# Kernel tuning notes

Measured on AMD Instinct MI355X. Metric: run time of the kernel, lower is better.

Reference implementation:

```python
import jax, jax.numpy as jnp
import numpy as np
import math

B, S, D = 4, 2048, 1024
H, HD, L = 16, 64, 512
ROPE_BASE = 10000.0
EPS = 1e-6


def _rope_angles(seq_len, head_dim, base):
    # (seq_len, head_dim//2) rotation angles
    inv_freq = 1.0 / (base ** (jnp.arange(0, head_dim, 2, dtype=jnp.float32) / head_dim))
    pos = jnp.arange(seq_len, dtype=jnp.float32)
    return pos[:, None] * inv_freq[None, :]


def _apply_rope(t, ang):
    # t: (B, H, S, HD); half-split rotation (rotate-half convention)
    cos = jnp.cos(ang)  # (S, HD//2)
    sin = jnp.sin(ang)
    t1, t2 = jnp.split(t, 2, axis=-1)
    return jnp.concatenate([t1 * cos - t2 * sin, t1 * sin + t2 * cos], axis=-1)


def setup_inputs() -> dict:
    key = jax.random.key(0)
    ks = jax.random.split(key, 7)
    def w(k, shape, fan_in):
        return jax.random.normal(k, shape, jnp.float32) * (fan_in ** -0.5)
    return {
        "x": jax.random.normal(ks[0], (B, S, D), jnp.float32),
        "norm_w": jnp.ones((D,), jnp.float32),
        "wq": w(ks[1], (D, H * HD), D),
        "kv_down": w(ks[2], (D, L), D),
        "wk": w(ks[3], (L, H * HD), L),
        "wv": w(ks[4], (L, H * HD), L),
        "wo": w(ks[5], (H * HD, D), H * HD),
    }


def reference(x, norm_w, wq, kv_down, wk, wv, wo):
    residual = x
    # RMSNorm
    var = jnp.mean(x * x, axis=-1, keepdims=True)
    xn = x * jax.lax.rsqrt(var + EPS) * norm_w
    # Projections: q from full x, k/v from latent down-projection
    q = (xn @ wq).reshape(B, S, H, HD).transpose(0, 2, 1, 3)          # (B,H,S,HD)
    kv = xn @ kv_down                                                  # (B,S,L)
    k = (kv @ wk).reshape(B, S, H, HD).transpose(0, 2, 1, 3)
    v = (kv @ wv).reshape(B, S, H, HD).transpose(0, 2, 1, 3)
    # RoPE
    ang = _rope_angles(S, HD, ROPE_BASE)
    q = _apply_rope(q, ang)
    k = _apply_rope(k, ang)
    # Attention (full, no mask)
    scale = 1.0 / math.sqrt(HD)
    attn = jnp.einsum("bhsd,bhtd->bhst", q, k) * scale
    attn = jax.nn.softmax(attn, axis=-1)
    out = jnp.einsum("bhst,bhtd->bhsd", attn, v)
    out = out.transpose(0, 2, 1, 3).reshape(B, S, H * HD) @ wo
    return residual + out
```

## Files before the change

### kernel.cpp

```cpp
#include <hip/hip_runtime.h>

typedef unsigned short u16;
typedef unsigned int   u32;
typedef __attribute__((ext_vector_type(8)))  __bf16 bf16x8;
typedef __attribute__((ext_vector_type(2)))  __bf16 bf16x2;
typedef __attribute__((ext_vector_type(8)))  short  short8;
typedef __attribute__((ext_vector_type(4)))  float  f32x4;
typedef __attribute__((ext_vector_type(16))) float  f32x16;
typedef __attribute__((ext_vector_type(4)))  u16    u16x4;
typedef __attribute__((ext_vector_type(4)))  u32    u32x4;

#define DEV static __device__ __forceinline__

DEV u16 f2bf(float f){ return __builtin_bit_cast(u16, (__bf16)f); }
DEV u32 pkbf(float a, float b){ bf16x2 t; t[0] = (__bf16)a; t[1] = (__bf16)b;
                                return __builtin_bit_cast(u32, t); }

#if __has_builtin(__builtin_amdgcn_exp2f)
DEV float fexp2(float x){ return __builtin_amdgcn_exp2f(x); }
#else
DEV float fexp2(float x){ return exp2f(x); }
#endif

DEV f32x4 mfma16(short8 a, short8 b, f32x4 c){
  return __builtin_amdgcn_mfma_f32_16x16x32_bf16(
      __builtin_bit_cast(bf16x8, a), __builtin_bit_cast(bf16x8, b), c, 0, 0, 0);
}
DEV f32x16 mfma32(short8 a, short8 b, f32x16 c){
  return __builtin_amdgcn_mfma_f32_32x32x16_bf16(
      __builtin_bit_cast(bf16x8, a), __builtin_bit_cast(bf16x8, b), c, 0, 0, 0);
}
DEV int swz(int byteoff, int row){ return byteoff ^ ((row & 7) << 4); }

#if __has_builtin(__builtin_amdgcn_global_load_lds)
#define USE_GLL 1
typedef __attribute__((address_space(1))) const u32 gas_u32;
typedef __attribute__((address_space(3)))       u32 las_u32;
#define GL2L(g, l) __builtin_amdgcn_global_load_lds((gas_u32*)(g), (las_u32*)(l), 16, 0, 0)
#define LSWZ(boff, r) swz(boff, r)
#else
#define LSWZ(boff, r) (boff)
#endif

__global__ __launch_bounds__(256) void k_prep(const float* __restrict__ wq,
                                              const float* __restrict__ kvd,
                                              const float* __restrict__ wk,
                                              const float* __restrict__ wv,
                                              const float* __restrict__ wo,
                                              const float* __restrict__ x,
                                              const float* __restrict__ norm_w,
                                              u16* __restrict__ wqT, u16* __restrict__ kvdT,
                                              u16* __restrict__ wkT, u16* __restrict__ wvT,
                                              u16* __restrict__ woT, u16* __restrict__ xn,
                                              float2* __restrict__ cs, float qscale){
  const int z = blockIdx.z;
  if (z == 6){
    const int bid = blockIdx.y*32 + blockIdx.x;
    const int t = threadIdx.x;
    __shared__ float ps[4];
    const float4 g = ((const float4*)norm_w)[t];
    #pragma unroll 1
    for (int it = 0; it < 8; ++it){
      const int row = bid*8 + it;
      const float4 v = ((const float4*)(x + (size_t)row*1024))[t];
      float ss = v.x*v.x + v.y*v.y + v.z*v.z + v.w*v.w;
      #pragma unroll
      for (int off=32; off; off>>=1) ss += __shfl_xor(ss, off, 64);
      if ((t & 63) == 0) ps[t>>6] = ss;
      __syncthreads();
      const float tot = ps[0]+ps[1]+ps[2]+ps[3];
      const float rinv = rsqrtf(tot * (1.0f/1024.0f) + 1e-6f);
      u16x4 o;
      o.x = f2bf(v.x*rinv*g.x); o.y = f2bf(v.y*rinv*g.y);
      o.z = f2bf(v.z*rinv*g.z); o.w = f2bf(v.w*rinv*g.w);
      *(u16x4*)(xn + (size_t)row*1024 + t*4) = o;
      __syncthreads();
    }
    return;
  }
  if (z == 5){
    if (blockIdx.y >= 8) return;
    const int idx = (blockIdx.y*32 + blockIdx.x)*256 + threadIdx.x;
    const int s = idx >> 5, j = idx & 31;
    const float ang = (float)s * expf(-(float)j * (9.210340371976184f/32.0f));
    cs[idx] = make_float2(cosf(ang), sinf(ang));
    return;
  }
  const float* W; u16* Wt; int K, N; float sc = 1.0f;
  switch (z){
    case 0: W = wq;  Wt = wqT;  K = 1024; N = 1024; sc = qscale; break;
    case 1: W = kvd; Wt = kvdT; K = 1024; N = 512;  break;
    case 2: W = wk;  Wt = wkT;  K = 512;  N = 1024; break;
    case 3: W = wv;  Wt = wvT;  K = 512;  N = 1024; break;
    default: W = wo; Wt = woT;  K = 1024; N = 1024; break;
  }
  const int k0 = blockIdx.x*32, n0 = blockIdx.y*32;
  if (k0 >= K || n0 >= N) return;
  __shared__ float t[32][33];
  const int tx = threadIdx.x & 31, ty = threadIdx.x >> 5;
  #pragma unroll
  for (int j=0;j<4;++j) t[ty + j*8][tx] = W[(size_t)(k0+ty+j*8)*N + n0 + tx];
  __syncthreads();
  #pragma unroll
  for (int j=0;j<4;++j) Wt[(size_t)(n0+ty+j*8)*K + k0 + tx] = f2bf(t[tx][ty+j*8]*sc);
}

template<int MODE>
__global__ __launch_bounds__(256) void k_gemm(const u16* __restrict__ A,
                                              const u16* __restrict__ Bt,
                                              const u16* __restrict__ Bt2,
                                              u16* __restrict__ Cb,
                                              u16* __restrict__ Cb2,
                                              float* __restrict__ Cf,
                                              const float* __restrict__ resid,
                                              const float2* __restrict__ cs,
                                              int K){
  __shared__ __align__(16) u16 Al[2][128*64];
  __shared__ __align__(16) u16 Bl[2][128*64];
  const int tid = threadIdx.x, lane = tid & 63, w = tid >> 6;
  const int wm = (w >> 1) * 64, wn = (w & 1) * 64;

  const int gx = gridDim.x;
  const int nwg = gx * gridDim.y;
  int fid = blockIdx.y * gx + blockIdx.x;
  fid = (fid & 7) * (nwg >> 3) + (fid >> 3);
  const int bx = fid % gx, by = fid / gx;

  const bool second = (MODE != 2) && (bx >= 8);
  const u16* B = second ? Bt2 : Bt;
  const int n0 = (second ? bx - 8 : bx) * 128;
  const int m0 = by * 128;
  const int lr = lane & 15, lg = lane >> 4;
  const int nt = K >> 6;

  f32x4 acc[4][4] = {};

#ifdef USE_GLL
  const int rin  = lane >> 3;
  const int colq = (lane & 7) ^ rin;
  auto stage = [&](int t_){
    u16* Ad = &Al[t_ & 1][0];
    u16* Bd = &Bl[t_ & 1][0];
    const int kb = t_ << 6;
    #pragma unroll
    for (int j=0;j<4;++j){
      const int c = w*4 + j;
      GL2L(A + (size_t)(m0 + c*8 + rin)*K + kb + colq*8, Ad + c*512);
      GL2L(B + (size_t)(n0 + c*8 + rin)*K + kb + colq*8, Bd + c*512);
    }
  };
#else
  auto stage = [&](int t_){
    u16* Ad = &Al[t_ & 1][0];
    u16* Bd = &Bl[t_ & 1][0];
    const int kb = t_ << 6;
    const int srow = tid >> 1, scol = (tid & 1) * 32;
    #pragma unroll
    for (int j=0;j<4;++j){
      *(short8*)(Ad + srow*64 + scol + j*8) = *(const short8*)(A + (size_t)(m0+srow)*K + kb + scol + j*8);
      *(short8*)(Bd + srow*64 + scol + j*8) = *(const short8*)(B + (size_t)(n0+srow)*K + kb + scol + j*8);
    }
  };
#endif

  stage(0);
  for (int t = 0; t < nt; ++t){
    __syncthreads();
    if (t + 1 < nt) stage(t + 1);
    const u16* Ab = &Al[t & 1][0];
    const u16* Bb = &Bl[t & 1][0];
    #pragma unroll
    for (int kk=0; kk<2; ++kk){
      const int cb = kk*64 + lg*16;
      short8 af[4], bfr[4];
      #pragma unroll
      for (int m=0;m<4;++m){
        const int r = wm + m*16 + lr;
        af[m] = *(const short8*)((const char*)Ab + LSWZ(r*128 + cb, r));
      }
      #pragma unroll
      for (int n=0;n<4;++n){
        const int r = wn + n*16 + lr;
        bfr[n] = *(const short8*)((const char*)Bb + LSWZ(r*128 + cb, r));
      }
      #pragma unroll
      for (int m=0;m<4;++m)
        #pragma unroll
        for (int n=0;n<4;++n)
          acc[m][n] = mfma16(af[m], bfr[n], acc[m][n]);
    }
  }

  #pragma unroll
  for (int m=0;m<4;++m){
    const int rb = m0 + wm + m*16 + lg*4;
    if (MODE == 2){
      #pragma unroll
      for (int n=0;n<4;++n){
        const int c = n0 + wn + n*16 + lr;
        #pragma unroll
        for (int i=0;i<4;++i){
          const size_t off = (size_t)(rb+i)*1024 + c;
          Cf[off] = acc[m][n][i] + resid[off];
        }
      }
    } else if (!second){
      #pragma unroll
      for (int n=0;n<2;++n){
        const int c = n0 + wn + n*16 + lr;
        const int j = n*16 + lr;
        #pragma unroll
        for (int i=0;i<4;++i){
          const float2 t = cs[(size_t)((rb+i) & 2047)*32 + j];
          const float t1 = acc[m][n][i], t2 = acc[m][n+2][i];
          Cb[(size_t)(rb+i)*1024 + c]      = f2bf(t1*t.x - t2*t.y);
          Cb[(size_t)(rb+i)*1024 + c + 32] = f2bf(t1*t.y + t2*t.x);
        }
      }
    } else if (MODE == 4){
      #pragma unroll
      for (int n=0;n<4;++n){
        const int c = n0 + wn + n*16 + lr;
        #pragma unroll
        for (int i=0;i<4;++i) Cb2[(size_t)(rb+i)*512 + c] = f2bf(acc[m][n][i]);
      }
    } else {
      #pragma unroll
      for (int n=0;n<4;++n){
        const int c = n0 + wn + n*16 + lr;
        const int b = rb >> 11, s = rb & 2047;
        u16x4 pk;
        pk.x = f2bf(acc[m][n][0]); pk.y = f2bf(acc[m][n][1]);
        pk.z = f2bf(acc[m][n][2]); pk.w = f2bf(acc[m][n][3]);
        *(u16x4*)(Cb2 + (((size_t)(b*1024 + c)) << 11) + s) = pk;
      }
    }
  }
}

__global__ __launch_bounds__(512, 4) void k_attn(const u16* __restrict__ q,
                                                 const u16* __restrict__ kmat,
                                                 const u16* __restrict__ vT,
                                                 u16* __restrict__ o){
  __shared__ __align__(16) u16 Kl[2][64*64];
  __shared__ __align__(16) u16 Vl[2][64*64];
  const int tid = threadIdx.x, lane = tid & 63, w = tid >> 6;
  const int l31 = lane & 31, hi = lane >> 5;

  const int fid = blockIdx.y * 8 + blockIdx.x;
  const int sid = (fid & 7) * 64 + (fid >> 3);
  const int qx = sid & 7, bh = sid >> 3;
  const int b = bh >> 4, h = bh & 15;
  const int q0 = qx * 256;

  short8 qf[4];
  {
    const size_t base = ((size_t)(b*2048 + q0 + w*32 + l31) << 10) + (h<<6) + hi*8;
    qf[0] = *(const short8*)(q + base);
    qf[1] = *(const short8*)(q + base + 16);
    qf[2] = *(const short8*)(q + base + 32);
    qf[3] = *(const short8*)(q + base + 48);
  }
  f32x16 oacc0 = {}, oacc1 = {};
  f32x16 accl  = {};
  float m = -1e30f;
  const short8 ones = {0x3F80,0x3F80,0x3F80,0x3F80,0x3F80,0x3F80,0x3F80,0x3F80};

  int roff[8];
  #pragma unroll
  for (int c=0;c<4;++c){
    roff[c*2+0] = swz(l31*128      + c*32 + hi*16, l31);
    roff[c*2+1] = swz((32+l31)*128 + c*32 + hi*16, 32+l31);
  }

  const int rin  = lane >> 3;
  const int colq = (lane & 7) ^ rin;
  const u16* kp0 = kmat + ((size_t)(b*2048 + w*8 + rin) << 10) + (h<<6) + colq*8;
  const u16* vp0 = vT + (((size_t)(b*1024 + h*64 + w*8 + rin)) << 11) + colq*8;
  u16* const Kd0 = Kl[0] + w*512;  u16* const Kd1 = Kl[1] + w*512;
  u16* const Vd0 = Vl[0] + w*512;  u16* const Vd1 = Vl[1] + w*512;

#ifdef USE_GLL
  #define STAGE(KD, VD) { GL2L(kp0, KD); GL2L(vp0, VD);                         \
      kp0 += 65536; vp0 += 64; }
#else
  #define STAGE(KD, VD) { *(short8*)(KD + lane*8) = *(const short8*)(kp0);      \
      *(short8*)(VD + lane*8) = *(const short8*)(vp0);                          \
      kp0 += 65536; vp0 += 64; }
#endif

  #define TILE(BOFF) {                                                          \
    f32x16 s0 = {}, s1 = {};                                                    \
    __builtin_amdgcn_s_setprio(1);                                              \
    _Pragma("unroll")                                                           \
    for (int c=0;c<4;++c){                                                      \
      short8 kf0 = *(const short8*)((const char*)Kl + roff[c*2+0] + BOFF);      \
      short8 kf1 = *(const short8*)((const char*)Kl + roff[c*2+1] + BOFF);      \
      s0 = mfma32(kf0, qf[c], s0);                                              \
      s1 = mfma32(kf1, qf[c], s1);                                              \
    }                                                                           \
    __builtin_amdgcn_s_setprio(0);                                              \
    float tmax = fmaxf(s0[0], s0[1]);                                           \
    _Pragma("unroll")                                                           \
    for (int r=1;r<8;++r) tmax = fmaxf(fmaxf(tmax, s0[2*r]), s0[2*r+1]);        \
    _Pragma("unroll")                                                           \
    for (int r=0;r<8;++r) tmax = fmaxf(fmaxf(tmax, s1[2*r]), s1[2*r+1]);        \
    tmax = fmaxf(tmax, __shfl_xor(tmax, 32, 64));                               \
    if (__any(tmax > m + 8.0f)){                                                \
      const float mn = fmaxf(m, tmax);                                          \
      const float corr = fexp2(m - mn);                                         \
      m = mn;                                                                   \
      _Pragma("unroll")                                                         \
      for (int reg=0; reg<16; ++reg){                                           \
        const int cq = (reg&3) + 8*(reg>>2) + 4*hi;                             \
        const float cr = __shfl(corr, cq, 64);                                  \
        oacc0[reg] *= cr; oacc1[reg] *= cr; accl[reg] *= cr;                    \
      }                                                                         \
    }                                                                           \
    u32 pk0[8], pk1[8];                                                         \
    _Pragma("unroll")                                                           \
    for (int a=0;a<4;++a){                                                      \
      _Pragma("unroll")                                                         \
      for (int e=0;e<2;++e){                                                    \
        float pa = fexp2(s0[a*4+e*2] - m), pb = fexp2(s0[a*4+e*2+1] - m);       \
        pk0[a*2+e] = pkbf(pa, pb);                                              \
        pa = fexp2(s1[a*4+e*2] - m); pb = fexp2(s1[a*4+e*2+1] - m);             \
        pk1[a*2+e] = pkbf(pa, pb);                                              \
      }                                                                         \
    }                                                                           \
    __builtin_amdgcn_s_setprio(1);                                              \
    _Pragma("unroll")                                                           \
    for (int c=0;c<4;++c){                                                      \
      u32* pks = (c < 2) ? pk0 : pk1;                                           \
      const int cc = c & 1;                                                     \
      u32 a0 = pks[(2*cc)*2+0], b0 = pks[(2*cc+1)*2+0];                         \
      u32 a1 = pks[(2*cc)*2+1], b1 = pks[(2*cc+1)*2+1];                         \
      asm volatile("v_permlane32_swap_b32 %0, %1" : "+v"(a0), "+v"(b0));        \
      asm volatile("v_permlane32_swap_b32 %0, %1" : "+v"(a1), "+v"(b1));        \
      u32x4 pfv; pfv.x = a0; pfv.y = a1; pfv.z = b0; pfv.w = b1;                \
      const short8 pf = __builtin_bit_cast(short8, pfv);                        \
      short8 vf0 = *(const short8*)((const char*)Vl + roff[c*2+0] + BOFF);      \
      short8 vf1 = *(const short8*)((const char*)Vl + roff[c*2+1] + BOFF);      \
      oacc0 = mfma32(pf, vf0, oacc0);                                           \
      oacc1 = mfma32(pf, vf1, oacc1);                                           \
      accl  = mfma32(pf, ones, accl);                                           \
    }                                                                           \
    __builtin_amdgcn_s_setprio(0);                                              \
  }

  STAGE(Kd0, Vd0);
  #pragma unroll 1
  for (int tt = 0; tt < 16; ++tt){
    __syncthreads();
    STAGE(Kd1, Vd1);
    TILE(0);
    __syncthreads();
    if (tt < 15) STAGE(Kd0, Vd0);
    TILE(8192);
  }

  #pragma unroll
  for (int reg=0; reg<16; ++reg){
    const int cq = (reg&3) + 8*(reg>>2) + 4*hi;
    const float lv = 1.0f / accl[reg];
    const size_t rowbase = ((size_t)(b*2048 + q0 + w*32 + cq) << 10) + (h<<6);
    o[rowbase + l31]      = f2bf(oacc0[reg] * lv);
    o[rowbase + 32 + l31] = f2bf(oacc1[reg] * lv);
  }
  #undef STAGE
  #undef TILE
}

extern "C" void kernel_launch(void* const* d_in, const int* in_sizes, int n_in,
                              void* d_out, int out_size, void* d_ws, size_t ws_size,
                              hipStream_t stream){
  const float* x      = (const float*)d_in[0];
  const float* norm_w = (const float*)d_in[1];
  const float* wq     = (const float*)d_in[2];
  const float* kvd    = (const float*)d_in[3];
  const float* wk     = (const float*)d_in[4];
  const float* wv     = (const float*)d_in[5];
  const float* wo     = (const float*)d_in[6];
  float* out = (float*)d_out;

  char* ws = (char*)d_ws;
  const size_t SZ = (size_t)8192*1024*2;
  u16* xn   = (u16*)(ws);
  u16* q    = (u16*)(ws + SZ);
  u16* kmat = (u16*)(ws + 2*SZ);
  u16* vT   = (u16*)(ws + 3*SZ);
  u16* attn = (u16*)(ws + 4*SZ);
  u16* kv   = (u16*)(ws + 5*SZ);
  u16* wqT  = (u16*)(ws + 5*SZ + (size_t)8192*512*2);
  u16* kvdT = wqT  + 1024*1024;
  u16* wkT  = kvdT + 512*1024;
  u16* wvT  = wkT  + 1024*512;
  u16* woT  = wvT  + 1024*512;
  float2* cs = (float2*)(woT + 1024*1024);

  const float QSCALE = 0.125f * 1.4426950408889634f;

  k_prep<<<dim3(32,32,7), 256, 0, stream>>>(wq, kvd, wk, wv, wo, x, norm_w,
                                            wqT, kvdT, wkT, wvT, woT, xn, cs, QSCALE);

  k_gemm<4><<<dim3(12,64), 256, 0, stream>>>(xn, wqT, kvdT, q, kv, nullptr, nullptr, cs, 1024);
  k_gemm<5><<<dim3(16,64), 256, 0, stream>>>(kv, wkT, wvT, kmat, vT, nullptr, nullptr, cs, 512);

  k_attn<<<dim3(8,64), 512, 0, stream>>>(q, kmat, vT, attn);

  k_gemm<2><<<dim3(8,64), 256, 0, stream>>>(attn, woT, nullptr, nullptr, nullptr, out, x, nullptr, 1024);
}
```

Baseline: 189.7 us.

## Split attention over KV halves and merge partials in a combine kernel

Each attention block now covers only half of the key/value sequence, which doubles the grid from 512 to 1024 blocks. Each block writes an unnormalised partial output plus its running max and row sum. A new combine kernel merges the two partials with log-sum-exp rescaling and normalises the result. This split-K scheme raises parallelism and GPU occupancy, at the cost of extra global traffic for the partial outputs, an additional kernel launch, and reusing the xn and kv workspace buffers as scratch.

```diff
diff --git a/kernel.cpp b/kernel.cpp
--- a/kernel.cpp
+++ b/kernel.cpp
@@ -13,6 +13,7 @@
 #define DEV static __device__ __forceinline__
 
 DEV u16 f2bf(float f){ return __builtin_bit_cast(u16, (__bf16)f); }
+DEV float bf2f(u16 h){ return __builtin_bit_cast(float, (u32)h << 16); }
 DEV u32 pkbf(float a, float b){ bf16x2 t; t[0] = (__bf16)a; t[1] = (__bf16)b;
                                 return __builtin_bit_cast(u32, t); }
 
@@ -241,15 +242,18 @@
 __global__ __launch_bounds__(512, 4) void k_attn(const u16* __restrict__ q,
                                                  const u16* __restrict__ kmat,
                                                  const u16* __restrict__ vT,
-                                                 u16* __restrict__ o){
+                                                 u16* __restrict__ o1,
+                                                 u16* __restrict__ o2,
+                                                 float* __restrict__ ml){
   __shared__ __align__(16) u16 Kl[2][64*64];
   __shared__ __align__(16) u16 Vl[2][64*64];
   const int tid = threadIdx.x, lane = tid & 63, w = tid >> 6;
   const int l31 = lane & 31, hi = lane >> 5;
 
-  const int fid = blockIdx.y * 8 + blockIdx.x;
-  const int sid = (fid & 7) * 64 + (fid >> 3);
-  const int qx = sid & 7, bh = sid >> 3;
+  const int fid = blockIdx.y * 16 + blockIdx.x;
+  const int sid = (fid & 7) * 128 + (fid >> 3);
+  const int bh = sid >> 4, rem = sid & 15;
+  const int qx = rem >> 1, half = rem & 1;
   const int b = bh >> 4, h = bh & 15;
   const int q0 = qx * 256;
 
@@ -275,8 +279,8 @@
 
   const int rin  = lane >> 3;
   const int colq = (lane & 7) ^ rin;
-  const u16* kp0 = kmat + ((size_t)(b*2048 + w*8 + rin) << 10) + (h<<6) + colq*8;
-  const u16* vp0 = vT + (((size_t)(b*1024 + h*64 + w*8 + rin)) << 11) + colq*8;
+  const u16* kp0 = kmat + ((size_t)(b*2048 + half*1024 + w*8 + rin) << 10) + (h<<6) + colq*8;
+  const u16* vp0 = vT + (((size_t)(b*1024 + h*64 + w*8 + rin)) << 11) + half*1024 + colq*8;
   u16* const Kd0 = Kl[0] + w*512;  u16* const Kd1 = Kl[1] + w*512;
   u16* const Vd0 = Vl[0] + w*512;  u16* const Vd1 = Vl[1] + w*512;
 
@@ -350,25 +354,56 @@
 
   STAGE(Kd0, Vd0);
   #pragma unroll 1
-  for (int tt = 0; tt < 16; ++tt){
+  for (int tt = 0; tt < 8; ++tt){
     __syncthreads();
     STAGE(Kd1, Vd1);
     TILE(0);
     __syncthreads();
-    if (tt < 15) STAGE(Kd0, Vd0);
+    if (tt < 7) STAGE(Kd0, Vd0);
     TILE(8192);
   }
 
+  u16* dst = half ? o2 : o1;
   #pragma unroll
   for (int reg=0; reg<16; ++reg){
     const int cq = (reg&3) + 8*(reg>>2) + 4*hi;
-    const float lv = 1.0f / accl[reg];
     const size_t rowbase = ((size_t)(b*2048 + q0 + w*32 + cq) << 10) + (h<<6);
-    o[rowbase + l31]      = f2bf(oacc0[reg] * lv);
-    o[rowbase + 32 + l31] = f2bf(oacc1[reg] * lv);
-  }
+    dst[rowbase + l31]      = f2bf(oacc0[reg]);
+    dst[rowbase + 32 + l31] = f2bf(oacc1[reg]);
+    if (l31 == 0)
+      ml[(((size_t)bh*2048) + q0 + w*32 + cq)*4 + 2*half + 1] = accl[reg];
+  }
+  if (hi == 0)
+    ml[(((size_t)bh*2048) + q0 + w*32 + l31)*4 + 2*half] = m;
   #undef STAGE
   #undef TILE
+}
+
+__global__ __launch_bounds__(256) void k_combine(u16* io1,
+                                                 const u16* __restrict__ o2,
+                                                 const float* __restrict__ ml){
+  const int idx = blockIdx.x*256 + threadIdx.x;
+  const int row = idx >> 7;
+  const int col = (idx & 127) * 8;
+  const int h = col >> 6;
+  const int b = row >> 11, s = row & 2047;
+  const size_t mlb = (((size_t)(b*16 + h))*2048 + s)*4;
+  const float m1 = ml[mlb],   l1 = ml[mlb+1];
+  const float m2 = ml[mlb+2], l2 = ml[mlb+3];
+  const float mm = fmaxf(m1, m2);
+  const float a1 = fexp2(m1 - mm), a2 = fexp2(m2 - mm);
+  const float inv = 1.0f / (a1*l1 + a2*l2);
+  const float f1 = a1*inv, f2 = a2*inv;
+  const size_t off = (size_t)row*1024 + col;
+  const short8 v1 = *(const short8*)(io1 + off);
+  const short8 v2 = *(const short8*)(o2 + off);
+  short8 ro;
+  #pragma unroll
+  for (int e=0;e<8;++e){
+    const float x = bf2f((u16)v1[e])*f1 + bf2f((u16)v2[e])*f2;
+    ro[e] = (short)f2bf(x);
+  }
+  *(short8*)(io1 + off) = ro;
 }
 
 extern "C" void kernel_launch(void* const* d_in, const int* in_sizes, int n_in,
@@ -397,6 +432,7 @@
   u16* wvT  = wkT  + 1024*512;
   u16* woT  = wvT  + 1024*512;
   float2* cs = (float2*)(woT + 1024*1024);
+  float* ml = (float*)kv;
 
   const float QSCALE = 0.125f * 1.4426950408889634f;
 
@@ -406,7 +442,8 @@
   k_gemm<4><<<dim3(12,64), 256, 0, stream>>>(xn, wqT, kvdT, q, kv, nullptr, nullptr, cs, 1024);
   k_gemm<5><<<dim3(16,64), 256, 0, stream>>>(kv, wkT, wvT, kmat, vT, nullptr, nullptr, cs, 512);
 
-  k_attn<<<dim3(8,64), 512, 0, stream>>>(q, kmat, vT, attn);
+  k_attn<<<dim3(16,64), 512, 0, stream>>>(q, kmat, vT, attn, xn, ml);
+  k_combine<<<4096, 256, 0, stream>>>(attn, xn, ml);
 
   k_gemm<2><<<dim3(8,64), 256, 0, stream>>>(attn, woT, nullptr, nullptr, nullptr, out, x, nullptr, 1024);
 }
```

After: 203.3 us. 7.2% more time.
